# Optimization experiments

Hardware: AMD Instinct MI355X
Metric: run time of the kernel (lower is better)

Reference implementation:

```python
import jax, jax.numpy as jnp
import numpy as np
from jax import lax

C = 128; H = 28; W = 28
VID_LENS = [32, 96, 64, 48, 80, 40, 88, 64]  # sums to 512
T_TOTAL = sum(VID_LENS)


def setup_inputs() -> dict:
    key = jax.random.key(0)
    ks = jax.random.split(key, 6)
    fan2 = C * 9
    fan1 = C * 3
    return {
        "x": jax.random.normal(ks[0], (T_TOTAL, C, H, W), dtype=jnp.float32),
        "vid_lens": jnp.array(VID_LENS, dtype=jnp.int32),
        "w_sp": jax.random.normal(ks[1], (C, C, 3, 3), dtype=jnp.float32) / np.sqrt(fan2),
        "b_sp": jax.random.normal(ks[2], (C,), dtype=jnp.float32) * 0.01,
        "w_t": jax.random.normal(ks[3], (C, C, 3), dtype=jnp.float32) / np.sqrt(fan1),
        "b_t": jax.random.normal(ks[4], (C,), dtype=jnp.float32) * 0.01,
        "alpha": jnp.full((C,), 0.25, dtype=jnp.float32),  # MultiNL ~ per-channel PReLU
    }


def _forward(x, vid_lens, w_sp, b_sp, w_t, b_t, alpha):
    projection = x
    # spatial 3x3 conv, stride 1, padding 1 (SAME), NCHW
    y = lax.conv_general_dilated(
        x, w_sp, window_strides=(1, 1), padding="SAME",
        dimension_numbers=("NCHW", "OIHW", "NCHW")) + b_sp[None, :, None, None]

    # Ragged temporal conv1d (k=3, pad=1) over concatenated time axis.
    # Zero the temporal neighbors at segment boundaries so each video is
    # convolved independently (equivalent to per-segment zero padding).
    T = y.shape[0]
    ends = jnp.cumsum(vid_lens)            # segment end indices (exclusive)
    starts = ends - vid_lens               # segment start indices
    start_mask = jnp.zeros((T,), bool).at[starts].set(True)
    end_mask = jnp.zeros((T,), bool).at[ends - 1].set(True)

    y_prev = jnp.where(start_mask[:, None, None, None], 0.0, jnp.roll(y, 1, axis=0))
    y_next = jnp.where(end_mask[:, None, None, None], 0.0, jnp.roll(y, -1, axis=0))

    # conv1d along time == per-tap channel-mixing matmul
    z = (jnp.einsum("oc,tchw->tohw", w_t[:, :, 0], y_prev)
         + jnp.einsum("oc,tchw->tohw", w_t[:, :, 1], y)
         + jnp.einsum("oc,tchw->tohw", w_t[:, :, 2], y_next)
         + b_t[None, :, None, None])

    # MultiNL modeled as per-channel PReLU
    z = jnp.where(z >= 0, z, alpha[None, :, None, None] * z)
    return z + projection


def reference(x, vid_lens, w_sp, b_sp, w_t, b_t, alpha):
    out = _forward(x, vid_lens, w_sp, b_sp, w_t, b_t, alpha)
    return (out, vid_lens)  # lengths are unchanged (k=3, pad=1)
```

## Files before the change

kernel.cpp:

```cpp
#include <hip/hip_runtime.h>

#define TT   512
#define CH   128
#define HWP  784
#define NSEG 8
#define NOUT 51380224

typedef short bf16x8  __attribute__((ext_vector_type(8)));
typedef float f32x4   __attribute__((ext_vector_type(4)));
typedef float f32x16  __attribute__((ext_vector_type(16)));
typedef int   i32x4   __attribute__((ext_vector_type(4)));
typedef unsigned short u16x4 __attribute__((ext_vector_type(4)));
typedef unsigned short u16x8 __attribute__((ext_vector_type(8)));

__device__ inline unsigned short f2bf(float f) {
    unsigned u = __builtin_bit_cast(unsigned, f);
    u += 0x7fffu + ((u >> 16) & 1u);
    return (unsigned short)(u >> 16);
}

__device__ inline void gld_lds16(const void* g, void* l) {
    __builtin_amdgcn_global_load_lds(
        (const __attribute__((address_space(1))) void*)g,
        (__attribute__((address_space(3))) void*)l, 16, 0, 0);
}

#define MFMA32(A, B, C) __builtin_amdgcn_mfma_f32_32x32x16_bf16(A, B, C, 0, 0, 0)

__global__ void repack_wsp(const float* __restrict__ w, short* __restrict__ wA) {
    int s = blockIdx.x * 256 + threadIdx.x;
    if (s >= 128 * 128 * 9) return;
    int co = s / 1152, r = s % 1152, ci = r / 9, kh = (r % 9) / 3, kw = r % 3;
    int tap = kh * 3 + kw;
    int m = co >> 5, row = co & 31;
    int ks = ci >> 4, kgrp = (ci >> 3) & 1, e = ci & 7;
    int lane = kgrp * 32 + row;
    int dst = (((tap * 8 + ks) * 4 + m) * 64 + lane) * 8 + e;
    wA[dst] = (short)f2bf(w[s]);
}

__global__ void repack_wt2(const float* __restrict__ w, short* __restrict__ wAt) {
    int s = blockIdx.x * 256 + threadIdx.x;
    if (s >= 128 * 128 * 3) return;
    int o = s / 384, r = s % 384, i = r / 3, tap = r % 3;
    int dst = tap * 16384 + (o >> 4) * 2048 + (i >> 5) * 512 +
              ((i >> 3) & 3) * 128 + (o & 15) * 8 + (i & 7);
    wAt[dst] = (short)f2bf(w[s]);
}

__global__ __launch_bounds__(512, 2) void spatial_mfma(
    const float* __restrict__ x, const short* __restrict__ wA,
    const float* __restrict__ b_sp, unsigned short* __restrict__ yT)
{
    __shared__ __align__(16) short xs[300 * 128];
    char* xsb = (char*)xs;
    const int t = blockIdx.y;
    const int r0 = blockIdx.x * 8;
    const int rows = (28 - r0 < 8) ? (28 - r0) : 8;
    const int pxcnt = rows * 28;
    const int tid = threadIdx.x;

    for (int u = tid; u < 4480; u += 512) {
        int cp = u & 63, q = u >> 6;
        int rl = q / 7, g = q % 7;
        int rr = r0 - 1 + rl;
        float4 f0 = make_float4(0.f, 0.f, 0.f, 0.f), f1 = f0;
        if (rr >= 0 && rr < 28) {
            const float* px0 = &x[((size_t)(t * CH + 2 * cp)) * HWP + rr * 28 + g * 4];
            f0 = *(const float4*)px0;
            f1 = *(const float4*)(px0 + HWP);
        }
        unsigned u0[4] = {__builtin_bit_cast(unsigned, f0.x), __builtin_bit_cast(unsigned, f0.y),
                          __builtin_bit_cast(unsigned, f0.z), __builtin_bit_cast(unsigned, f0.w)};
        unsigned u1[4] = {__builtin_bit_cast(unsigned, f1.x), __builtin_bit_cast(unsigned, f1.y),
                          __builtin_bit_cast(unsigned, f1.z), __builtin_bit_cast(unsigned, f1.w)};
        int stb = rl * 30 + g * 4 + 1;
#pragma unroll
        for (int j = 0; j < 4; ++j) {
            int st = stb + j;
            unsigned val = __builtin_amdgcn_perm(u1[j], u0[j], 0x07060302u);
            int addr = (st << 8) | (((cp >> 2) ^ (st & 15)) << 4) | ((cp & 3) << 2);
            *(unsigned*)(xsb + addr) = val;
        }
    }
    for (int v = tid; v < 1280; v += 512) {
        int cp = v & 63, k = v >> 6;
        int st = (k >> 1) * 30 + (k & 1) * 29;
        int addr = (st << 8) | (((cp >> 2) ^ (st & 15)) << 4) | ((cp & 3) << 2);
        *(unsigned*)(xsb + addr) = 0u;
    }
    __syncthreads();

    const int wid = tid >> 6, l = tid & 63;
    const int l31 = l & 31, bb5 = l >> 5;
    const int ch = wid & 1, pg = wid >> 1;
    const int ch2 = ch * 2;
    const int tI0 = pg * 2, tI1 = pg * 2 + 1;

    const int p0 = tI0 * 32 + l31;
    const int p1 = tI1 * 32 + l31;
    const bool ok1t = (tI1 < 7);
    const int pc0 = (p0 < pxcnt) ? p0 : 0;
    const int pc1 = (ok1t && p1 < pxcnt) ? p1 : 0;
    const int st0_0 = (pc0 / 28 + 1) * 30 + pc0 % 28 + 1;
    const int st0_1 = (pc1 / 28 + 1) * 30 + pc1 % 28 + 1;

    f32x16 zz = {};
    f32x16 acc00 = zz, acc10 = zz;
    f32x16 acc01 = zz, acc11 = zz;

    const bf16x8* wv = (const bf16x8*)wA;

    for (int tap = 0; tap < 9; ++tap) {
        const int off = (tap / 3 - 1) * 30 + (tap % 3) - 1;
        const int stv0 = st0_0 + off, stv1 = st0_1 + off;
        const int rb0 = stv0 << 8, sw0 = stv0 & 15;
        const int rb1 = stv1 << 8, sw1 = stv1 & 15;

        bf16x8 A[16];
#pragma unroll
        for (int k2 = 0; k2 < 16; ++k2)
            A[k2] = wv[((tap * 8 + (k2 >> 1)) * 4 + ch2 + (k2 & 1)) * 64 + l];
        i32x4 B0[8], B1[8];
#pragma unroll
        for (int ks = 0; ks < 8; ++ks) {
            B0[ks] = *(const i32x4*)(xsb + (rb0 | (((ks * 2 + bb5) ^ sw0) << 4)));
            B1[ks] = *(const i32x4*)(xsb + (rb1 | (((ks * 2 + bb5) ^ sw1) << 4)));
        }
        __builtin_amdgcn_sched_barrier(0);
        asm volatile("s_waitcnt vmcnt(0) lgkmcnt(0)" ::: "memory");
        __builtin_amdgcn_sched_barrier(0);
        __builtin_amdgcn_s_setprio(1);
#pragma unroll
        for (int ks = 0; ks < 8; ++ks) {
            bf16x8 f0 = __builtin_bit_cast(bf16x8, B0[ks]);
            bf16x8 f1 = __builtin_bit_cast(bf16x8, B1[ks]);
            acc00 = MFMA32(A[ks * 2],     f0, acc00);
            acc10 = MFMA32(A[ks * 2 + 1], f0, acc10);
            acc01 = MFMA32(A[ks * 2],     f1, acc01);
            acc11 = MFMA32(A[ks * 2 + 1], f1, acc11);
        }
        __builtin_amdgcn_s_setprio(0);
        __builtin_amdgcn_sched_barrier(0);
    }

    __syncthreads();
    const int wbase = wid * 8704;
#pragma unroll
    for (int mi = 0; mi < 2; ++mi) {
#pragma unroll
        for (int r2 = 0; r2 < 4; ++r2) {
            int cb = (ch2 + mi) * 32 + 8 * r2 + 4 * bb5;
            float4 bs = *(const float4*)&b_sp[cb];
            float bsa[4] = {bs.x, bs.y, bs.z, bs.w};
            u16x4 k0, k1;
#pragma unroll
            for (int q = 0; q < 4; ++q) {
                k0[q] = f2bf((mi ? acc10[r2 * 4 + q] : acc00[r2 * 4 + q]) + bsa[q]);
                k1[q] = f2bf((mi ? acc11[r2 * 4 + q] : acc01[r2 * 4 + q]) + bsa[q]);
            }
            int co_off = (mi * 32 + 8 * r2 + 4 * bb5) * 2;
            *(u16x4*)(xsb + wbase + l31 * 136 + co_off) = k0;
            *(u16x4*)(xsb + wbase + 4352 + l31 * 136 + co_off) = k1;
        }
    }
#pragma unroll
    for (int tt2 = 0; tt2 < 2; ++tt2) {
        int tI = tt2 ? tI1 : tI0;
#pragma unroll
        for (int j = 0; j < 4; ++j) {
            int idx = j * 64 + l;
            int pxl = idx >> 3, sub = idx & 7;
            u16x8 v = *(const u16x8*)(xsb + wbase + tt2 * 4352 + pxl * 136 + sub * 16);
            int p = tI * 32 + pxl;
            if (tI < 7 && p < pxcnt) {
                char* dst = (char*)yT + ((size_t)t * HWP + r0 * 28 + p) * 256 +
                            ch * 128 + sub * 16;
                *(u16x8*)dst = v;
            }
        }
    }
}

__global__ __launch_bounds__(256, 4) void temporal_mfma(
    const unsigned short* __restrict__ yT, const short* __restrict__ wAt,
    const float* __restrict__ b_t, const float* __restrict__ alpha,
    const float* __restrict__ x, const int* __restrict__ vid_lens,
    float* __restrict__ out)
{
    __shared__ __align__(16) char ldsT[29696];

    const int chunk = blockIdx.x, t = blockIdx.y;
    const int tid = threadIdx.x, wid = tid >> 6, l = tid & 63;
    const int l15 = l & 15, kgrp = l >> 4;
    const int sx = l15 & 7;

    bool isS = false, isE = false;
    {
        int cum = 0;
        for (int s = 0; s < NSEG; ++s) {
            if (t == cum) isS = true;
            cum += vid_lens[s];
            if (t == cum - 1) isE = true;
        }
    }
    const bool tapAct[3] = {!isS, true, !isE};

    auto stage = [&](int s) {
        int tap = s >> 1, kp = s & 1;
        if (!tapAct[tap]) return;
        int tp = t + tap - 1;
        const char* yb = (const char*)yT + (size_t)tp * HWP * 256;
        char* buf = ldsT + (s & 1) * 14336;
#pragma unroll
        for (int r = 0; r < 4; ++r) {
            int c = r * 256 + wid * 64 + l;
            if (r < 3 || wid < 2) {
                int px = c >> 3, sp = c & 7;
                int ssrc = sp ^ (px & 7);
                const char* g = yb + ((size_t)(chunk * 112 + px)) * 256 + kp * 128 + ssrc * 16;
                char* ldst = buf + (r * 256 + wid * 64) * 16;
                gld_lds16(g, ldst);
            }
        }
    };

    f32x4 acc[2][7];
#pragma unroll
    for (int m = 0; m < 2; ++m)
#pragma unroll
        for (int n = 0; n < 7; ++n) acc[m][n] = (f32x4){0.f, 0.f, 0.f, 0.f};

    const bf16x8* wAv = (const bf16x8*)wAt;

    stage(0);
    __syncthreads();

    for (int s = 0; s < 6; ++s) {
        if (s < 5) stage(s + 1);
        int tap = s >> 1, kp = s & 1;
        if (tapAct[tap]) {
            const char* buf = ldsT + (s & 1) * 14336;
            bf16x8 a[2][2];
#pragma unroll
            for (int m = 0; m < 2; ++m)
#pragma unroll
                for (int k1 = 0; k1 < 2; ++k1)
                    a[m][k1] = wAv[((tap * 8 + wid * 2 + m) * 4 + kp * 2 + k1) * 64 + l];
            __builtin_amdgcn_s_setprio(1);
#pragma unroll
            for (int k1 = 0; k1 < 2; ++k1) {
#pragma unroll
                for (int nf = 0; nf < 7; ++nf) {
                    int addr = (nf * 16 + l15) * 128 + ((k1 * 4 + kgrp) ^ sx) * 16;
                    i32x4 bi = *(const i32x4*)(buf + addr);
                    bf16x8 b = __builtin_bit_cast(bf16x8, bi);
                    acc[0][nf] = __builtin_amdgcn_mfma_f32_16x16x32_bf16(a[0][k1], b, acc[0][nf], 0, 0, 0);
                    acc[1][nf] = __builtin_amdgcn_mfma_f32_16x16x32_bf16(a[1][k1], b, acc[1][nf], 0, 0, 0);
                }
            }
            __builtin_amdgcn_s_setprio(0);
        }
        __syncthreads();
    }

    float* fl = (float*)ldsT;
    const int wbase = wid * 1856;
#pragma unroll
    for (int m = 0; m < 2; ++m) {
#pragma unroll
        for (int nf = 0; nf < 7; ++nf)
#pragma unroll
            for (int rr = 0; rr < 4; ++rr)
                fl[wbase + (kgrp * 4 + rr) * 116 + nf * 16 + l15] = acc[m][nf][rr];
#pragma unroll
        for (int j = 0; j < 7; ++j) {
            int idx = j * 64 + l;
            int co_r = idx / 28, q = idx % 28;
            f32x4 v4 = *(const f32x4*)&fl[wbase + co_r * 116 + q * 4];
            int co_g = wid * 32 + m * 16 + co_r;
            float bt = b_t[co_g], al = alpha[co_g];
            size_t gi = ((size_t)(t * CH + co_g)) * HWP + chunk * 112 + q * 4;
            float4 xv = *(const float4*)&x[gi];
            float xr[4] = {xv.x, xv.y, xv.z, xv.w};
            float rrv[4];
#pragma unroll
            for (int e = 0; e < 4; ++e) {
                float v = v4[e] + bt;
                v = (v >= 0.f) ? v : al * v;
                rrv[e] = v + xr[e];
            }
            *(float4*)&out[gi] = make_float4(rrv[0], rrv[1], rrv[2], rrv[3]);
        }
        __syncthreads();
    }
}

__global__ void write_lens(const int* __restrict__ vid_lens, float* __restrict__ out) {
    int i = threadIdx.x;
    if (i < NSEG) out[NOUT + i] = (float)vid_lens[i];
}

extern "C" void kernel_launch(void* const* d_in, const int* in_sizes, int n_in,
                              void* d_out, int out_size, void* d_ws, size_t ws_size,
                              hipStream_t stream) {
    const float* x        = (const float*)d_in[0];
    const int*   vid_lens = (const int*)d_in[1];
    const float* w_sp     = (const float*)d_in[2];
    const float* b_sp     = (const float*)d_in[3];
    const float* w_t      = (const float*)d_in[4];
    const float* b_t      = (const float*)d_in[5];
    const float* alpha    = (const float*)d_in[6];
    float* out = (float*)d_out;

    unsigned short* yT = (unsigned short*)d_ws;
    short* wA  = (short*)((char*)d_ws + 102760448);
    short* wAt = (short*)((char*)d_ws + 102760448 + 294912);

    repack_wsp<<<576, 256, 0, stream>>>(w_sp, wA);
    repack_wt2<<<192, 256, 0, stream>>>(w_t, wAt);
    spatial_mfma<<<dim3(4, 512), 512, 0, stream>>>(x, wA, b_sp, yT);
    temporal_mfma<<<dim3(7, 512), 256, 0, stream>>>(yT, wAt, b_t, alpha, x, vid_lens, out);
    write_lens<<<1, 64, 0, stream>>>(vid_lens, out);
}
```

Baseline: 371.7 us.

## Software-pipeline weight loads across half-taps with double-buffered registers

Splits each tap's weight fragment loads into two halves, held in two register sets, and issues them with inline-asm global loads one half ahead of use. Partial vmcnt waits then let the MFMAs of one half run while the next half's weights are still in flight, instead of waiting for every load at each tap. This targets the global-load latency stall that precedes each tap's MFMA block. It fully unrolls the tap loop and keeps 16 A vectors live, which raises register pressure, and it depends on hand-counted waitcnt values being correct.

```diff
diff --git a/kernel.cpp b/kernel.cpp
--- a/kernel.cpp
+++ b/kernel.cpp
@@ -26,6 +26,11 @@
 }
 
 #define MFMA32(A, B, C) __builtin_amdgcn_mfma_f32_32x32x16_bf16(A, B, C, 0, 0, 0)
+#define BC8(x) __builtin_bit_cast(bf16x8, x)
+
+__device__ __forceinline__ i32x4 ldB(const char* xsb, int rb, int sw, int slot) {
+    return *(const i32x4*)(xsb + (rb | ((slot ^ sw) << 4)));
+}
 
 __global__ void repack_wsp(const float* __restrict__ w, short* __restrict__ wA) {
     int s = blockIdx.x * 256 + threadIdx.x;
@@ -47,6 +52,54 @@
               ((i >> 3) & 3) * 128 + (o & 15) * 8 + (i & 7);
     wAt[dst] = (short)f2bf(w[s]);
 }
+
+#define ISSUE_A(HH, R0, R1, R2, R3, R4, R5, R6, R7) do {                         \
+    const char* pA_ = wAl + ((HH) >> 1) * 32768 + ((HH) & 1) * 16384;            \
+    const char* pB_ = pA_ + 4096;                                                \
+    const char* pC_ = pA_ + 8192;                                                \
+    const char* pD_ = pA_ + 12288;                                               \
+    asm volatile("global_load_dwordx4 %0, %1, off"             : "=v"(R0) : "v"(pA_)); \
+    asm volatile("global_load_dwordx4 %0, %1, off offset:1024" : "=v"(R1) : "v"(pA_)); \
+    asm volatile("global_load_dwordx4 %0, %1, off"             : "=v"(R2) : "v"(pB_)); \
+    asm volatile("global_load_dwordx4 %0, %1, off offset:1024" : "=v"(R3) : "v"(pB_)); \
+    asm volatile("global_load_dwordx4 %0, %1, off"             : "=v"(R4) : "v"(pC_)); \
+    asm volatile("global_load_dwordx4 %0, %1, off offset:1024" : "=v"(R5) : "v"(pC_)); \
+    asm volatile("global_load_dwordx4 %0, %1, off"             : "=v"(R6) : "v"(pD_)); \
+    asm volatile("global_load_dwordx4 %0, %1, off offset:1024" : "=v"(R7) : "v"(pD_)); \
+} while (0)
+
+#define HALF_BODY(LASTWAIT, HODD, R0, R1, R2, R3, R4, R5, R6, R7) do {           \
+    i32x4 b00 = ldB(xsb, rb0, sw0, (HODD) * 8 + 0 + bb5);                        \
+    i32x4 b01 = ldB(xsb, rb0, sw0, (HODD) * 8 + 2 + bb5);                        \
+    i32x4 b02 = ldB(xsb, rb0, sw0, (HODD) * 8 + 4 + bb5);                        \
+    i32x4 b03 = ldB(xsb, rb0, sw0, (HODD) * 8 + 6 + bb5);                        \
+    i32x4 b10 = ldB(xsb, rb1, sw1, (HODD) * 8 + 0 + bb5);                        \
+    i32x4 b11 = ldB(xsb, rb1, sw1, (HODD) * 8 + 2 + bb5);                        \
+    i32x4 b12 = ldB(xsb, rb1, sw1, (HODD) * 8 + 4 + bb5);                        \
+    i32x4 b13 = ldB(xsb, rb1, sw1, (HODD) * 8 + 6 + bb5);                        \
+    if (LASTWAIT) { asm volatile("s_waitcnt vmcnt(0) lgkmcnt(0)" ::: "memory"); }\
+    else          { asm volatile("s_waitcnt vmcnt(8) lgkmcnt(0)" ::: "memory"); }\
+    __builtin_amdgcn_sched_barrier(0);                                           \
+    __builtin_amdgcn_s_setprio(1);                                               \
+    acc00 = MFMA32(BC8(R0), BC8(b00), acc00);                                    \
+    acc10 = MFMA32(BC8(R1), BC8(b00), acc10);                                    \
+    acc01 = MFMA32(BC8(R0), BC8(b10), acc01);                                    \
+    acc11 = MFMA32(BC8(R1), BC8(b10), acc11);                                    \
+    acc00 = MFMA32(BC8(R2), BC8(b01), acc00);                                    \
+    acc10 = MFMA32(BC8(R3), BC8(b01), acc10);                                    \
+    acc01 = MFMA32(BC8(R2), BC8(b11), acc01);                                    \
+    acc11 = MFMA32(BC8(R3), BC8(b11), acc11);                                    \
+    acc00 = MFMA32(BC8(R4), BC8(b02), acc00);                                    \
+    acc10 = MFMA32(BC8(R5), BC8(b02), acc10);                                    \
+    acc01 = MFMA32(BC8(R4), BC8(b12), acc01);                                    \
+    acc11 = MFMA32(BC8(R5), BC8(b12), acc11);                                    \
+    acc00 = MFMA32(BC8(R6), BC8(b03), acc00);                                    \
+    acc10 = MFMA32(BC8(R7), BC8(b03), acc10);                                    \
+    acc01 = MFMA32(BC8(R6), BC8(b13), acc01);                                    \
+    acc11 = MFMA32(BC8(R7), BC8(b13), acc11);                                    \
+    __builtin_amdgcn_s_setprio(0);                                               \
+    __builtin_amdgcn_sched_barrier(0);                                           \
+} while (0)
 
 __global__ __launch_bounds__(512, 2) void spatial_mfma(
     const float* __restrict__ x, const short* __restrict__ wA,
@@ -109,39 +162,25 @@
     f32x16 acc00 = zz, acc10 = zz;
     f32x16 acc01 = zz, acc11 = zz;
 
-    const bf16x8* wv = (const bf16x8*)wA;
-
+    const char* wAl = (const char*)wA + ch2 * 1024 + l * 16;
+
+    i32x4 A00, A01, A02, A03, A04, A05, A06, A07;
+    i32x4 A10, A11, A12, A13, A14, A15, A16, A17;
+    ISSUE_A(0, A00, A01, A02, A03, A04, A05, A06, A07);
+    ISSUE_A(1, A10, A11, A12, A13, A14, A15, A16, A17);
+
+#pragma unroll
     for (int tap = 0; tap < 9; ++tap) {
         const int off = (tap / 3 - 1) * 30 + (tap % 3) - 1;
         const int stv0 = st0_0 + off, stv1 = st0_1 + off;
         const int rb0 = stv0 << 8, sw0 = stv0 & 15;
         const int rb1 = stv1 << 8, sw1 = stv1 & 15;
 
-        bf16x8 A[16];
-#pragma unroll
-        for (int k2 = 0; k2 < 16; ++k2)
-            A[k2] = wv[((tap * 8 + (k2 >> 1)) * 4 + ch2 + (k2 & 1)) * 64 + l];
-        i32x4 B0[8], B1[8];
-#pragma unroll
-        for (int ks = 0; ks < 8; ++ks) {
-            B0[ks] = *(const i32x4*)(xsb + (rb0 | (((ks * 2 + bb5) ^ sw0) << 4)));
-            B1[ks] = *(const i32x4*)(xsb + (rb1 | (((ks * 2 + bb5) ^ sw1) << 4)));
-        }
-        __builtin_amdgcn_sched_barrier(0);
-        asm volatile("s_waitcnt vmcnt(0) lgkmcnt(0)" ::: "memory");
-        __builtin_amdgcn_sched_barrier(0);
-        __builtin_amdgcn_s_setprio(1);
-#pragma unroll
-        for (int ks = 0; ks < 8; ++ks) {
-            bf16x8 f0 = __builtin_bit_cast(bf16x8, B0[ks]);
-            bf16x8 f1 = __builtin_bit_cast(bf16x8, B1[ks]);
-            acc00 = MFMA32(A[ks * 2],     f0, acc00);
-            acc10 = MFMA32(A[ks * 2 + 1], f0, acc10);
-            acc01 = MFMA32(A[ks * 2],     f1, acc01);
-            acc11 = MFMA32(A[ks * 2 + 1], f1, acc11);
-        }
-        __builtin_amdgcn_s_setprio(0);
-        __builtin_amdgcn_sched_barrier(0);
+        HALF_BODY(false, 0, A00, A01, A02, A03, A04, A05, A06, A07);
+        if (tap < 8) ISSUE_A(2 * tap + 2, A00, A01, A02, A03, A04, A05, A06, A07);
+
+        HALF_BODY(tap == 8, 1, A10, A11, A12, A13, A14, A15, A16, A17);
+        if (tap < 8) ISSUE_A(2 * tap + 3, A10, A11, A12, A13, A14, A15, A16, A17);
     }
 
     __syncthreads();
```

Measured after the change: 361.0 us. 2.9% less time.

## Stage spatial conv weights into double-buffered LDS via async global-to-LDS loads

Applied to the files above, without the earlier changes.

Weight fragments for each 3x3 tap are no longer loaded per-wave from global memory into registers. They are now staged once per block into a double-buffered LDS region with global_load_lds, and the next tap is prefetched while the current tap's MFMAs run. The full unrolled register preload and explicit waitcnt give way to interleaved per-ks LDS reads, with a barrier after each tap. LDS use grows to about 140KB, which allows only one block per CU, so the launch_bounds occupancy hint of 2 is dropped. The barrier relies on the compiler inserting a vmcnt wait for the async loads, and the extra syncs and lower occupancy could offset the reduced redundant global weight traffic.

```diff
diff --git a/kernel.cpp b/kernel.cpp
--- a/kernel.cpp
+++ b/kernel.cpp
@@ -26,6 +26,11 @@
 }
 
 #define MFMA32(A, B, C) __builtin_amdgcn_mfma_f32_32x32x16_bf16(A, B, C, 0, 0, 0)
+#define BC8(x) __builtin_bit_cast(bf16x8, x)
+
+__device__ __forceinline__ i32x4 ldB(const char* xsb, int rb, int sw, int slot) {
+    return *(const i32x4*)(xsb + (rb | ((slot ^ sw) << 4)));
+}
 
 __global__ void repack_wsp(const float* __restrict__ w, short* __restrict__ wA) {
     int s = blockIdx.x * 256 + threadIdx.x;
@@ -48,12 +53,13 @@
     wAt[dst] = (short)f2bf(w[s]);
 }
 
-__global__ __launch_bounds__(512, 2) void spatial_mfma(
+__global__ __launch_bounds__(512) void spatial_mfma(
     const float* __restrict__ x, const short* __restrict__ wA,
     const float* __restrict__ b_sp, unsigned short* __restrict__ yT)
 {
-    __shared__ __align__(16) short xs[300 * 128];
-    char* xsb = (char*)xs;
+    __shared__ __align__(16) char lds_all[76800 + 2 * 32768];
+    char* xsb = lds_all;
+    char* abufs = lds_all + 76800;
     const int t = blockIdx.y;
     const int r0 = blockIdx.x * 8;
     const int rows = (28 - r0 < 8) ? (28 - r0) : 8;
@@ -89,6 +95,17 @@
         int addr = (st << 8) | (((cp >> 2) ^ (st & 15)) << 4) | ((cp & 3) << 2);
         *(unsigned*)(xsb + addr) = 0u;
     }
+
+    const int wuni = (tid & ~63) * 16;
+    auto stageA = [&](int tap, int s) {
+        char* ab = abufs + s * 32768;
+#pragma unroll
+        for (int k = 0; k < 4; ++k) {
+            const char* g = (const char*)wA + tap * 32768 + (k * 512 + tid) * 16;
+            gld_lds16(g, ab + k * 8192 + wuni);
+        }
+    };
+    stageA(0, 0);
     __syncthreads();
 
     const int wid = tid >> 6, l = tid & 63;
@@ -109,42 +126,34 @@
     f32x16 acc00 = zz, acc10 = zz;
     f32x16 acc01 = zz, acc11 = zz;
 
-    const bf16x8* wv = (const bf16x8*)wA;
-
+    const int l16 = l << 4;
+
+#pragma unroll
     for (int tap = 0; tap < 9; ++tap) {
+        if (tap < 8) stageA(tap + 1, (tap + 1) & 1);
+
         const int off = (tap / 3 - 1) * 30 + (tap % 3) - 1;
         const int stv0 = st0_0 + off, stv1 = st0_1 + off;
         const int rb0 = stv0 << 8, sw0 = stv0 & 15;
         const int rb1 = stv1 << 8, sw1 = stv1 & 15;
-
-        bf16x8 A[16];
-#pragma unroll
-        for (int k2 = 0; k2 < 16; ++k2)
-            A[k2] = wv[((tap * 8 + (k2 >> 1)) * 4 + ch2 + (k2 & 1)) * 64 + l];
-        i32x4 B0[8], B1[8];
+        const char* ab = abufs + (tap & 1) * 32768;
+
 #pragma unroll
         for (int ks = 0; ks < 8; ++ks) {
-            B0[ks] = *(const i32x4*)(xsb + (rb0 | (((ks * 2 + bb5) ^ sw0) << 4)));
-            B1[ks] = *(const i32x4*)(xsb + (rb1 | (((ks * 2 + bb5) ^ sw1) << 4)));
-        }
-        __builtin_amdgcn_sched_barrier(0);
-        asm volatile("s_waitcnt vmcnt(0) lgkmcnt(0)" ::: "memory");
-        __builtin_amdgcn_sched_barrier(0);
-        __builtin_amdgcn_s_setprio(1);
-#pragma unroll
-        for (int ks = 0; ks < 8; ++ks) {
-            bf16x8 f0 = __builtin_bit_cast(bf16x8, B0[ks]);
-            bf16x8 f1 = __builtin_bit_cast(bf16x8, B1[ks]);
-            acc00 = MFMA32(A[ks * 2],     f0, acc00);
-            acc10 = MFMA32(A[ks * 2 + 1], f0, acc10);
-            acc01 = MFMA32(A[ks * 2],     f1, acc01);
-            acc11 = MFMA32(A[ks * 2 + 1], f1, acc11);
-        }
-        __builtin_amdgcn_s_setprio(0);
-        __builtin_amdgcn_sched_barrier(0);
-    }
-
-    __syncthreads();
+            i32x4 a0 = *(const i32x4*)(ab + (ks * 4 + ch2) * 1024 + l16);
+            i32x4 a1 = *(const i32x4*)(ab + (ks * 4 + ch2 + 1) * 1024 + l16);
+            i32x4 b0 = ldB(xsb, rb0, sw0, ks * 2 + bb5);
+            i32x4 b1 = ldB(xsb, rb1, sw1, ks * 2 + bb5);
+            __builtin_amdgcn_s_setprio(1);
+            acc00 = MFMA32(BC8(a0), BC8(b0), acc00);
+            acc10 = MFMA32(BC8(a1), BC8(b0), acc10);
+            acc01 = MFMA32(BC8(a0), BC8(b1), acc01);
+            acc11 = MFMA32(BC8(a1), BC8(b1), acc11);
+            __builtin_amdgcn_s_setprio(0);
+        }
+        __syncthreads();
+    }
+
     const int wbase = wid * 8704;
 #pragma unroll
     for (int mi = 0; mi < 2; ++mi) {
```

Result: faster. 333.6 us (-10.3%).
